# Optimization experiments

Hardware: AMD Instinct MI355X
Metric: run time of the kernel (lower is better)

## Reference

```python
import jax, jax.numpy as jnp
import numpy as np

# Fixed generation configuration (original samples num_nodes per graph from
# dataset stats; here batched with fixed node count so shapes are static).
B, N = 64, 384                 # num_graphs, nodes per graph
NOISE, CED, HID, FEAT, NCLS = 128, 64, 512, 256, 10
DENSITY = 0.05                 # fallback density used by the original code
TEMP = 1.0                     # temperature
IU, JU = np.triu_indices(N, k=1)   # all i<j pairs, matches nested loop order
P = IU.shape[0]                # pairs per graph = N*(N-1)/2
K = int(round(DENSITY * P))    # topk edges per graph


def setup_inputs() -> dict:
    key = jax.random.key(0)
    ks = jax.random.split(key, 8)
    f32 = jnp.float32
    return {
        "z": jax.random.normal(ks[0], (B, N, NOISE), f32),
        "class_labels": jax.random.randint(ks[1], (B,), 0, NCLS),
        "embed_table": jax.random.normal(ks[2], (NCLS, CED), f32),
        "W1": jax.random.normal(ks[3], (NOISE + CED, HID), f32) / np.float32(np.sqrt(NOISE + CED)),
        "b1": jnp.zeros((HID,), f32),
        "W2": jax.random.normal(ks[4], (HID, FEAT), f32) / np.float32(np.sqrt(HID)),
        "b2": jnp.zeros((FEAT,), f32),
        "We": jax.random.normal(ks[5], (FEAT, HID), f32) / np.float32(np.sqrt(FEAT)),
        "be": jnp.zeros((HID,), f32),
        "threshold": jnp.float32(1.0),
    }


def reference(z, class_labels, embed_table, W1, b1, W2, b2, We, be, threshold):
    # class embedding, broadcast to every node of the graph
    ce = embed_table[class_labels]                               # [B, CED]
    ce = jnp.broadcast_to(ce[:, None, :], (B, N, CED))
    inp = jnp.concatenate([z, ce], axis=-1)                      # [B, N, NOISE+CED]
    # node generator: Linear -> ReLU -> Linear
    x = jax.nn.relu(inp @ W1 + b1) @ W2 + b2                     # [B, N, FEAT]
    # edge predictor encoder: Linear -> ReLU
    h = jax.nn.relu(x @ We + be)                                 # [B, N, HID]
    # pairwise L2 distances via gram trick (replaces O(n^2) torch.norm loop)
    sq = jnp.sum(h * h, axis=-1)                                 # [B, N]
    gram = jnp.einsum('bnd,bmd->bnm', h, h)                      # [B, N, N]
    d2 = jnp.maximum(sq[:, :, None] + sq[:, None, :] - 2.0 * gram, 0.0)
    dist = jnp.sqrt(jnp.maximum(d2[:, IU, JU], 1e-12))           # [B, P] upper-tri pairs
    probs = jax.nn.sigmoid((threshold - dist) / max(TEMP, 1e-6)) # [B, P]
    # per-graph top-k edge selection
    top_probs, top_idx = jax.lax.top_k(probs, K)                 # [B, K]
    iu = jnp.asarray(IU, jnp.int32)
    ju = jnp.asarray(JU, jnp.int32)
    offs = (jnp.arange(B, dtype=jnp.int32) * N)[:, None]         # node offset per graph
    u = iu[top_idx] + offs                                       # [B, K]
    v = ju[top_idx] + offs
    # per graph: [[u, v], [v, u]] (symmetrized), graphs concatenated
    row0 = jnp.concatenate([u, v], axis=1).reshape(-1)           # [B*2K]
    row1 = jnp.concatenate([v, u], axis=1).reshape(-1)
    edge_index = jnp.stack([row0, row1], axis=0)                 # [2, B*2K]
    batch = jnp.repeat(jnp.arange(B, dtype=jnp.int32), N)        # [B*N]
    return x.reshape(B * N, FEAT), edge_index, batch, top_probs
```

## Files before the change

### kernel.cpp

```cpp
#include <hip/hip_runtime.h>
#include <hip/hip_bf16.h>

#define NB    64
#define NN    384
#define PPAIR 73536
#define PRECT 147456
#define KSEL  3677
#define NSLICE 8
#define SLICEK (PRECT / NSLICE)

#define OFF_X 0
#define OFF_E 6291456
#define B2K   470656
#define OFF_B 7232768
#define OFF_P 7257344
#define TOT   7492672

#define WS_H8    0ull
#define WS_GH    0ull
#define WS_SB    4194304ull
#define WS_SQ    12582912ull
#define WS_W1P   12681216ull
#define WS_W2P   12877824ull
#define WS_WEP   13139968ull
#define WS_KEY   13402112ull
#define WS_TB    39509248ull

typedef __attribute__((ext_vector_type(8))) short bf16x8;
typedef __attribute__((ext_vector_type(4))) float f32x4;

__device__ __forceinline__ short f2bf(float f) {
    __hip_bfloat16 h = __float2bfloat16(f);
    return *reinterpret_cast<short*>(&h);
}
__device__ __forceinline__ unsigned enc8(float h) {
    if (!(h > 0.0078125f)) return 0u;
    unsigned u = __float_as_uint(h) + 0x00080000u;
    int E = (int)(u >> 23) - 127;
    if (E > 8)  return 0x7Eu;
    if (E < -6) return 0u;
    return (unsigned)(((E + 7) << 3) | ((u >> 20) & 7u));
}
__device__ __forceinline__ float dec8(unsigned b) {
    if (b == 0u) return 0.f;
    return __uint_as_float((((b >> 3) + 120u) << 23) | ((b & 7u) << 20));
}

__device__ __forceinline__ void bar_lds() {
    asm volatile("s_waitcnt lgkmcnt(0)\n\ts_barrier" ::: "memory");
}

__device__ __forceinline__ int2 pack4bf(float a, float b, float c, float d) {
    int2 pk;
    pk.x = (unsigned short)f2bf(a) | ((unsigned)(unsigned short)f2bf(b) << 16);
    pk.y = (unsigned short)f2bf(c) | ((unsigned)(unsigned short)f2bf(d) << 16);
    return pk;
}

__device__ __forceinline__ void packOne(
    const float* __restrict__ W, int K, int N, short* __restrict__ dst, int idx)
{
    if (idx >= K * N) return;
    int j = idx & 7;
    int l = (idx >> 3) & 63;
    int rest = idx >> 9;
    int Kt = K >> 5;
    int kt = rest % Kt, mt = rest / Kt;
    int k = kt * 32 + (l >> 4) * 8 + j;
    int n = mt * 16 + (l & 15);
    dst[idx] = f2bf(W[(size_t)k * N + n]);
}

__global__ __launch_bounds__(256) void pack_all_kernel(
    const float* __restrict__ W1, const float* __restrict__ W2,
    const float* __restrict__ We, short* __restrict__ W1p,
    short* __restrict__ W2p, short* __restrict__ Wep, float* __restrict__ sqW)
{
    int blk = blockIdx.x, tid = threadIdx.x;
    if (blk < 384)        packOne(W1, 192, 512, W1p, blk * 256 + tid);
    else if (blk < 896)   packOne(W2, 512, 256, W2p, (blk - 384) * 256 + tid);
    else if (blk < 1408)  packOne(We, 256, 512, Wep, (blk - 896) * 256 + tid);
    else {
        int i = (blk - 1408) * 256 + tid;
        if (i < NB * NN) sqW[i] = 0.f;
    }
}

__global__ __launch_bounds__(512, 6) void fused_mlp_kernel(
    const float* __restrict__ z, const int* __restrict__ cls,
    const float* __restrict__ et,
    const short* __restrict__ W1p, const float* __restrict__ b1,
    const short* __restrict__ W2p, const float* __restrict__ b2,
    const short* __restrict__ Wep, const float* __restrict__ be,
    float* __restrict__ xOut, unsigned char* __restrict__ h8Out,
    float* __restrict__ sqOut)
{
    __shared__ short lds[23040];
    short* A_lds  = lds;
    short* t1_lds = lds + 6400;
    short* x_lds  = lds;

    const int tid = threadIdx.x;
    const int r0 = blockIdx.x * 32;
    const int lane = tid & 63;
    const int l15 = lane & 15, kj = lane >> 4;
    const int w = tid >> 6;
    const int cl = cls[r0 / NN];

    {
        float4 v[3];
#pragma unroll
        for (int q = 0; q < 3; ++q) {
            int u = tid + q * 512;
            int row = u / 48, c4 = u - row * 48;
            int col = c4 * 4;
            const float* src = (col < 128)
                ? (z + (size_t)(r0 + row) * 128 + col)
                : (et + cl * 64 + (col - 128));
            v[q] = *(const float4*)src;
        }
#pragma unroll
        for (int q = 0; q < 3; ++q) {
            int u = tid + q * 512;
            int row = u / 48, c4 = u - row * 48;
            *(int2*)(A_lds + row * 200 + c4 * 4) =
                pack4bf(v[q].x, v[q].y, v[q].z, v[q].w);
        }
    }
    bar_lds();

    {
        f32x4 acc1[4][2];
#pragma unroll
        for (int m = 0; m < 4; ++m)
#pragma unroll
            for (int s = 0; s < 2; ++s) acc1[m][s] = (f32x4){0.f, 0.f, 0.f, 0.f};

#pragma unroll
        for (int kt = 0; kt < 6; ++kt) {
            bf16x8 bF[2];
#pragma unroll
            for (int s = 0; s < 2; ++s)
                bF[s] = *(const bf16x8*)(A_lds + (s * 16 + l15) * 200 + kt * 32 + (kj << 3));
#pragma unroll
            for (int m = 0; m < 4; ++m) {
                int mt = w * 4 + m;
                bf16x8 aF = *(const bf16x8*)(W1p + ((size_t)(mt * 6 + kt) << 9) + (lane << 3));
#pragma unroll
                for (int s = 0; s < 2; ++s)
                    acc1[m][s] = __builtin_amdgcn_mfma_f32_16x16x32_bf16(aF, bF[s], acc1[m][s], 0, 0, 0);
            }
        }
#pragma unroll
        for (int m = 0; m < 4; ++m) {
            int fl = (w * 4 + m) * 16 + (kj << 2);
            float4 bv = *(const float4*)(b1 + fl);
#pragma unroll
            for (int s = 0; s < 2; ++s) {
                int node = s * 16 + l15;
                f32x4 a = acc1[m][s];
                float v0 = fmaxf(a.x + bv.x, 0.f), v1 = fmaxf(a.y + bv.y, 0.f);
                float v2 = fmaxf(a.z + bv.z, 0.f), v3 = fmaxf(a.w + bv.w, 0.f);
                *(int2*)(t1_lds + node * 520 + fl) = pack4bf(v0, v1, v2, v3);
            }
        }
    }
    bar_lds();

    f32x4 acc2[2][2];
#pragma unroll
    for (int t = 0; t < 2; ++t)
#pragma unroll
        for (int s = 0; s < 2; ++s) acc2[t][s] = (f32x4){0.f, 0.f, 0.f, 0.f};

#pragma unroll
    for (int kt = 0; kt < 16; ++kt) {
        bf16x8 bF[2];
#pragma unroll
        for (int s = 0; s < 2; ++s)
            bF[s] = *(const bf16x8*)(t1_lds + (s * 16 + l15) * 520 + kt * 32 + (kj << 3));
#pragma unroll
        for (int t = 0; t < 2; ++t) {
            int mt = w * 2 + t;
            bf16x8 aF = *(const bf16x8*)(W2p + ((size_t)(mt * 16 + kt) << 9) + (lane << 3));
#pragma unroll
            for (int s = 0; s < 2; ++s)
                acc2[t][s] = __builtin_amdgcn_mfma_f32_16x16x32_bf16(aF, bF[s], acc2[t][s], 0, 0, 0);
        }
    }
    bar_lds();

#pragma unroll
    for (int t = 0; t < 2; ++t) {
        int feat = (w * 2 + t) * 16 + (kj << 2);
        float4 bv = *(const float4*)(b2 + feat);
#pragma unroll
        for (int s = 0; s < 2; ++s) {
            int node = s * 16 + l15;
            f32x4 a = acc2[t][s];
            float v0 = a.x + bv.x, v1 = a.y + bv.y;
            float v2 = a.z + bv.z, v3 = a.w + bv.w;
            float4 o; o.x = v0; o.y = v1; o.z = v2; o.w = v3;
            *(float4*)(xOut + (size_t)(r0 + node) * 256 + feat) = o;
            *(int2*)(x_lds + node * 264 + feat) = pack4bf(v0, v1, v2, v3);
        }
    }
    bar_lds();

    {
        f32x4 acc3[4][2];
#pragma unroll
        for (int m = 0; m < 4; ++m)
#pragma unroll
            for (int s = 0; s < 2; ++s) acc3[m][s] = (f32x4){0.f, 0.f, 0.f, 0.f};

#pragma unroll
        for (int kt = 0; kt < 8; ++kt) {
            bf16x8 bF[2];
#pragma unroll
            for (int s = 0; s < 2; ++s)
                bF[s] = *(const bf16x8*)(x_lds + (s * 16 + l15) * 264 + kt * 32 + (kj << 3));
#pragma unroll
            for (int m = 0; m < 4; ++m) {
                int mt = w * 4 + m;
                bf16x8 aF = *(const bf16x8*)(Wep + ((size_t)(mt * 8 + kt) << 9) + (lane << 3));
#pragma unroll
                for (int s = 0; s < 2; ++s)
                    acc3[m][s] = __builtin_amdgcn_mfma_f32_16x16x32_bf16(aF, bF[s], acc3[m][s], 0, 0, 0);
            }
        }
        float sqp[2] = {0.f, 0.f};
#pragma unroll
        for (int m = 0; m < 4; ++m) {
            int feat = (w * 4 + m) * 16 + (kj << 2);
            float4 bv = *(const float4*)(be + feat);
#pragma unroll
            for (int s = 0; s < 2; ++s) {
                int node = s * 16 + l15;
                f32x4 a = acc3[m][s];
                float v0 = fmaxf(a.x + bv.x, 0.f), v1 = fmaxf(a.y + bv.y, 0.f);
                float v2 = fmaxf(a.z + bv.z, 0.f), v3 = fmaxf(a.w + bv.w, 0.f);
                unsigned e0 = enc8(v0), e1 = enc8(v1), e2 = enc8(v2), e3 = enc8(v3);
                *(unsigned*)(h8Out + (size_t)(r0 + node) * 512 + feat) =
                    e0 | (e1 << 8) | (e2 << 16) | (e3 << 24);
                float h0 = dec8(e0), h1 = dec8(e1), h2 = dec8(e2), h3 = dec8(e3);
                sqp[s] += h0 * h0 + h1 * h1 + h2 * h2 + h3 * h3;
            }
        }
#pragma unroll
        for (int s = 0; s < 2; ++s) {
            float v = sqp[s];
            v += __shfl_xor(v, 16);
            v += __shfl_xor(v, 32);
            if (kj == 0)
                atomicAdd(sqOut + r0 + s * 16 + l15, v);
        }
    }
}

__global__ __launch_bounds__(256) void gram_mfma_kernel(
    const unsigned char* __restrict__ hW8, const float* __restrict__ sqW,
    unsigned short* __restrict__ keyW)
{
    extern __shared__ unsigned char smem8[];
    unsigned char* As = smem8;
    unsigned char* Bs = smem8 + 16896;

    const int tid = threadIdx.x;
    const int b  = blockIdx.x;
    int tp = blockIdx.y;
    int ti = 0; { int rem = tp; while (rem >= 6 - ti) { rem -= 6 - ti; ++ti; } tp = rem; }
    const int tj = ti + tp;
    const bool diag = (ti == tj);
    const unsigned char* Bp = diag ? As : Bs;

    const int w = tid >> 6;
    const int lane = tid & 63;
    const int l15 = lane & 15, kj = lane >> 4;
    const int mb = w * 16;

    f32x4 acc[4];
#pragma unroll
    for (int t = 0; t < 4; ++t) acc[t] = (f32x4){0.f, 0.f, 0.f, 0.f};

    const size_t baseA = ((size_t)b * NN + ti * 64) * 512;
    const size_t baseB = ((size_t)b * NN + tj * 64) * 512;

    int4 pa[4], pb[4];
    auto issue = [&](int kc) {
#pragma unroll
        for (int q = 0; q < 4; ++q) {
            int i = tid + (q << 8);
            int row = i >> 4, g = i & 15;
            pa[q] = *(const int4*)(hW8 + baseA + row * 512 + kc * 256 + g * 16);
            if (!diag)
                pb[q] = *(const int4*)(hW8 + baseB + row * 512 + kc * 256 + g * 16);
        }
    };
    auto store = [&]() {
#pragma unroll
        for (int q = 0; q < 4; ++q) {
            int i = tid + (q << 8);
            int row = i >> 4, g = i & 15;
            *(int4*)(As + row * 264 + g * 16) = pa[q];
            if (!diag) *(int4*)(Bs + row * 264 + g * 16) = pb[q];
        }
    };

    issue(0);
    for (int kc = 0; kc < 2; ++kc) {
        store();
        if (kc == 0) issue(1);
        bar_lds();
#pragma unroll
        for (int kt = 0; kt < 8; ++kt) {
            long long aF = *(const long long*)(As + (mb + l15) * 264 + kt * 32 + kj * 8);
#pragma unroll
            for (int nt = 0; nt < 4; ++nt) {
                long long bF = *(const long long*)(Bp + (nt * 16 + l15) * 264 + kt * 32 + kj * 8);
                acc[nt] = __builtin_amdgcn_mfma_f32_16x16x32_fp8_fp8(aF, bF, acc[nt], 0, 0, 0);
            }
        }
        bar_lds();
    }

    unsigned short* tile = (unsigned short*)smem8;
    float4 sqi = *(const float4*)(sqW + b * NN + ti * 64 + mb + kj * 4);
    float si[4] = { sqi.x, sqi.y, sqi.z, sqi.w };
#pragma unroll
    for (int nt = 0; nt < 4; ++nt) {
        int colL = nt * 16 + l15;
        float sj = sqW[b * NN + tj * 64 + colL];
        float av[4] = { acc[nt].x, acc[nt].y, acc[nt].z, acc[nt].w };
#pragma unroll
        for (int r = 0; r < 4; ++r) {
            int rowL = mb + kj * 4 + r;
            float d2 = fmaxf(si[r] + sj - 2.f * av[r], 0.f);
            unsigned short key = (unsigned short)(__float_as_uint(d2) >> 16);
            bool valid = !diag || (rowL < colL);
            tile[rowL * 72 + colL] = valid ? key : (unsigned short)0xFFFF;
        }
    }
    bar_lds();
#pragma unroll
    for (int it = 0; it < 2; ++it) {
        int idx = tid + (it << 8);
        int row = idx >> 3, c8 = idx & 7;
        int4 v = *(const int4*)(tile + row * 72 + c8 * 8);
        *(int4*)(keyW + (size_t)b * PRECT + (size_t)(ti * 64 + row) * NN
                 + tj * 64 + c8 * 8) = v;
    }
}

__global__ __launch_bounds__(1024) void selA_kernel(
    const unsigned short* __restrict__ keyW, unsigned short* __restrict__ ghist)
{
    const int b = blockIdx.x, s = blockIdx.y, tid = threadIdx.x;
    const unsigned short* keys = keyW + (size_t)b * PRECT + (size_t)s * SLICEK;
    __shared__ unsigned hist[4096];
    for (int i = tid; i < 4096; i += 1024) hist[i] = 0;
    __syncthreads();
    for (int p = tid; p < SLICEK; p += 1024) {
        unsigned k = keys[p];
        if (k < 0x8000u) atomicAdd(&hist[k >> 4], 1u);
    }
    __syncthreads();
    unsigned short* dst = ghist + ((size_t)(b * NSLICE + s) << 12);
    for (int i = tid; i < 4096; i += 1024) dst[i] = (unsigned short)hist[i];
}

__global__ __launch_bounds__(1024) void selB_kernel(
    const unsigned short* __restrict__ ghist, unsigned* __restrict__ sliceBase,
    unsigned* __restrict__ Tbuf, float* __restrict__ outF)
{
    const int b = blockIdx.x, tid = threadIdx.x;
    __shared__ unsigned base[4096];
    __shared__ unsigned scanBuf[1024];
    __shared__ int sTc;
    if (tid == 0) sTc = 4095;

    unsigned c[4]; unsigned tsum = 0;
#pragma unroll
    for (int q = 0; q < 4; ++q) {
        int bin = tid * 4 + q;
        unsigned v = 0;
        for (int s = 0; s < NSLICE; ++s)
            v += ghist[((size_t)(b * NSLICE + s) << 12) + bin];
        c[q] = v; tsum += v;
    }
    scanBuf[tid] = tsum;
    __syncthreads();
    for (int o = 1; o < 1024; o <<= 1) {
        unsigned v = (tid >= o) ? scanBuf[tid - o] : 0u;
        __syncthreads();
        scanBuf[tid] += v;
        __syncthreads();
    }
    unsigned exc = scanBuf[tid] - tsum;
    {
        unsigned run = exc;
#pragma unroll
        for (int q = 0; q < 4; ++q) { base[tid * 4 + q] = run; run += c[q]; }
    }
    __syncthreads();
#pragma unroll
    for (int q = 0; q < 4; ++q) {
        int i = tid * 4 + q;
        if (base[i] < KSEL && base[i] + c[q] >= KSEL) atomicMin(&sTc, i);
    }
    __syncthreads();
    if (tid == 0) Tbuf[b] = (unsigned)sTc;

#pragma unroll
    for (int q = 0; q < 4; ++q) {
        int bin = tid * 4 + q;
        unsigned runb = base[bin];
        for (int s = 0; s < NSLICE; ++s) {
            size_t off = ((size_t)(b * NSLICE + s) << 12) + bin;
            sliceBase[off] = runb;
            runb += ghist[off];
        }
    }
    for (int i = tid; i < NN; i += 1024)
        outF[OFF_B + (size_t)b * NN + i] = (float)b;
}

__global__ __launch_bounds__(1024) void selC_emit_kernel(
    const unsigned short* __restrict__ keyW, const unsigned* __restrict__ sliceBase,
    const unsigned* __restrict__ Tbuf, const float* __restrict__ thrp,
    float* __restrict__ outF)
{
    const int b = blockIdx.x, s = blockIdx.y, tid = threadIdx.x;
    const unsigned short* keys = keyW + (size_t)b * PRECT + (size_t)s * SLICEK;
    __shared__ unsigned cnt[4096];
    const unsigned* src = sliceBase + ((size_t)(b * NSLICE + s) << 12);
    for (int i = tid; i < 4096; i += 1024) cnt[i] = src[i];
    __syncthreads();
    const int T = (int)Tbuf[b];
    const float thr0 = thrp[0];
    float* eb = outF + OFF_E + (size_t)b * (2 * KSEL);
    for (int p = tid; p < SLICEK; p += 1024) {
        unsigned k = keys[p];
        if (k < 0x8000u) {
            int bin = k >> 4;
            if (bin <= T) {
                unsigned pos = atomicAdd(&cnt[bin], 1u);
                if (pos < KSEL) {
                    int pg = s * SLICEK + p;
                    int i = pg / NN;
                    int j = pg - i * NN;
                    float u = (float)(b * NN + i);
                    float v = (float)(b * NN + j);
                    eb[pos] = u;
                    eb[KSEL + pos] = v;
                    eb[B2K + pos] = v;
                    eb[B2K + KSEL + pos] = u;
                    float d2 = __uint_as_float(((unsigned)k) << 16);
                    float dist = sqrtf(fmaxf(d2, 1e-12f));
                    outF[OFF_P + (size_t)b * KSEL + pos] =
                        1.0f / (1.0f + expf(dist - thr0));
                }
            }
        }
    }
}

extern "C" void kernel_launch(void* const* d_in, const int* in_sizes, int n_in,
                              void* d_out, int out_size, void* d_ws, size_t ws_size,
                              hipStream_t stream) {
    (void)in_sizes; (void)n_in; (void)out_size; (void)ws_size;
    const float* z   = (const float*)d_in[0];
    const int*   cls = (const int*)d_in[1];
    const float* et  = (const float*)d_in[2];
    const float* W1  = (const float*)d_in[3];
    const float* b1  = (const float*)d_in[4];
    const float* W2  = (const float*)d_in[5];
    const float* b2  = (const float*)d_in[6];
    const float* We  = (const float*)d_in[7];
    const float* be  = (const float*)d_in[8];
    const float* thr = (const float*)d_in[9];
    float* outF = (float*)d_out;

    char* w = (char*)d_ws;
    unsigned char*  hW8   = (unsigned char*)(w + WS_H8);
    float*          sqW   = (float*)(w + WS_SQ);
    short*          W1p   = (short*)(w + WS_W1P);
    short*          W2p   = (short*)(w + WS_W2P);
    short*          Wep   = (short*)(w + WS_WEP);
    unsigned short* keyW  = (unsigned short*)(w + WS_KEY);
    unsigned short* ghist = (unsigned short*)(w + WS_GH);
    unsigned*       sbase = (unsigned*)(w + WS_SB);
    unsigned*       Tbuf  = (unsigned*)(w + WS_TB);

    pack_all_kernel<<<1504, 256, 0, stream>>>(W1, W2, We, W1p, W2p, Wep, sqW);

    fused_mlp_kernel<<<768, 512, 0, stream>>>(
        z, cls, et, W1p, b1, W2p, b2, Wep, be, outF + OFF_X, hW8, sqW);

    gram_mfma_kernel<<<dim3(64, 21), 256, 33792, stream>>>(hW8, sqW, keyW);
    selA_kernel<<<dim3(64, NSLICE), 1024, 0, stream>>>(keyW, ghist);
    selB_kernel<<<64, 1024, 0, stream>>>(ghist, sbase, Tbuf, outF);
    selC_emit_kernel<<<dim3(64, NSLICE), 1024, 0, stream>>>(
        keyW, sbase, Tbuf, thr, outF);
}
```

Baseline: 201.4 us.

## Fuse histogram build into gram kernel and use global per-graph bin counters

```diff
diff --git a/kernel.cpp b/kernel.cpp
--- a/kernel.cpp
+++ b/kernel.cpp
@@ -17,14 +17,14 @@
 #define TOT   7492672
 
 #define WS_H8    0ull
-#define WS_GH    0ull
-#define WS_SB    4194304ull
 #define WS_SQ    12582912ull
 #define WS_W1P   12681216ull
 #define WS_W2P   12877824ull
 #define WS_WEP   13139968ull
 #define WS_KEY   13402112ull
-#define WS_TB    39509248ull
+#define WS_GH32  32276480ull
+#define WS_GC    33325056ull
+#define WS_TB    34373632ull
 
 typedef __attribute__((ext_vector_type(8))) short bf16x8;
 typedef __attribute__((ext_vector_type(4))) float f32x4;
@@ -74,15 +74,19 @@
 __global__ __launch_bounds__(256) void pack_all_kernel(
     const float* __restrict__ W1, const float* __restrict__ W2,
     const float* __restrict__ We, short* __restrict__ W1p,
-    short* __restrict__ W2p, short* __restrict__ Wep, float* __restrict__ sqW)
+    short* __restrict__ W2p, short* __restrict__ Wep,
+    float* __restrict__ sqW, unsigned* __restrict__ ghist32)
 {
     int blk = blockIdx.x, tid = threadIdx.x;
     if (blk < 384)        packOne(W1, 192, 512, W1p, blk * 256 + tid);
     else if (blk < 896)   packOne(W2, 512, 256, W2p, (blk - 384) * 256 + tid);
     else if (blk < 1408)  packOne(We, 256, 512, Wep, (blk - 896) * 256 + tid);
-    else {
+    else if (blk < 1504) {
         int i = (blk - 1408) * 256 + tid;
         if (i < NB * NN) sqW[i] = 0.f;
+    } else {
+        int i = (blk - 1504) * 256 + tid;
+        if (i < NB * 4096) ghist32[i] = 0u;
     }
 }
 
@@ -260,7 +264,7 @@
 
 __global__ __launch_bounds__(256) void gram_mfma_kernel(
     const unsigned char* __restrict__ hW8, const float* __restrict__ sqW,
-    unsigned short* __restrict__ keyW)
+    unsigned short* __restrict__ keyW, unsigned* __restrict__ ghist32)
 {
     extern __shared__ unsigned char smem8[];
     unsigned char* As = smem8;
@@ -325,6 +329,10 @@
     }
 
     unsigned short* tile = (unsigned short*)smem8;
+    unsigned* hist = (unsigned*)(smem8 + 16896);
+    for (int i = tid; i < 4096; i += 256) hist[i] = 0;
+    bar_lds();
+
     float4 sqi = *(const float4*)(sqW + b * NN + ti * 64 + mb + kj * 4);
     float si[4] = { sqi.x, sqi.y, sqi.z, sqi.w };
 #pragma unroll
@@ -339,6 +347,8 @@
             unsigned short key = (unsigned short)(__float_as_uint(d2) >> 16);
             bool valid = !diag || (rowL < colL);
             tile[rowL * 72 + colL] = valid ? key : (unsigned short)0xFFFF;
+            if (valid && key < (unsigned short)0x8000u)
+                atomicAdd(&hist[key >> 4], 1u);
         }
     }
     bar_lds();
@@ -350,27 +360,14 @@
         *(int4*)(keyW + (size_t)b * PRECT + (size_t)(ti * 64 + row) * NN
                  + tj * 64 + c8 * 8) = v;
     }
-}
-
-__global__ __launch_bounds__(1024) void selA_kernel(
-    const unsigned short* __restrict__ keyW, unsigned short* __restrict__ ghist)
-{
-    const int b = blockIdx.x, s = blockIdx.y, tid = threadIdx.x;
-    const unsigned short* keys = keyW + (size_t)b * PRECT + (size_t)s * SLICEK;
-    __shared__ unsigned hist[4096];
-    for (int i = tid; i < 4096; i += 1024) hist[i] = 0;
-    __syncthreads();
-    for (int p = tid; p < SLICEK; p += 1024) {
-        unsigned k = keys[p];
-        if (k < 0x8000u) atomicAdd(&hist[k >> 4], 1u);
-    }
-    __syncthreads();
-    unsigned short* dst = ghist + ((size_t)(b * NSLICE + s) << 12);
-    for (int i = tid; i < 4096; i += 1024) dst[i] = (unsigned short)hist[i];
+    for (int i = tid; i < 4096; i += 256) {
+        unsigned v = hist[i];
+        if (v) atomicAdd(&ghist32[(size_t)b * 4096 + i], v);
+    }
 }
 
 __global__ __launch_bounds__(1024) void selB_kernel(
-    const unsigned short* __restrict__ ghist, unsigned* __restrict__ sliceBase,
+    const unsigned* __restrict__ ghist32, unsigned* __restrict__ gcnt,
     unsigned* __restrict__ Tbuf, float* __restrict__ outF)
 {
     const int b = blockIdx.x, tid = threadIdx.x;
@@ -383,9 +380,7 @@
 #pragma unroll
     for (int q = 0; q < 4; ++q) {
         int bin = tid * 4 + q;
-        unsigned v = 0;
-        for (int s = 0; s < NSLICE; ++s)
-            v += ghist[((size_t)(b * NSLICE + s) << 12) + bin];
+        unsigned v = ghist32[(size_t)b * 4096 + bin];
         c[q] = v; tsum += v;
     }
     scanBuf[tid] = tsum;
@@ -414,30 +409,22 @@
 #pragma unroll
     for (int q = 0; q < 4; ++q) {
         int bin = tid * 4 + q;
-        unsigned runb = base[bin];
-        for (int s = 0; s < NSLICE; ++s) {
-            size_t off = ((size_t)(b * NSLICE + s) << 12) + bin;
-            sliceBase[off] = runb;
-            runb += ghist[off];
-        }
+        gcnt[(size_t)b * 4096 + bin] = base[bin];
     }
     for (int i = tid; i < NN; i += 1024)
         outF[OFF_B + (size_t)b * NN + i] = (float)b;
 }
 
 __global__ __launch_bounds__(1024) void selC_emit_kernel(
-    const unsigned short* __restrict__ keyW, const unsigned* __restrict__ sliceBase,
+    const unsigned short* __restrict__ keyW, unsigned* __restrict__ gcnt,
     const unsigned* __restrict__ Tbuf, const float* __restrict__ thrp,
     float* __restrict__ outF)
 {
     const int b = blockIdx.x, s = blockIdx.y, tid = threadIdx.x;
     const unsigned short* keys = keyW + (size_t)b * PRECT + (size_t)s * SLICEK;
-    __shared__ unsigned cnt[4096];
-    const unsigned* src = sliceBase + ((size_t)(b * NSLICE + s) << 12);
-    for (int i = tid; i < 4096; i += 1024) cnt[i] = src[i];
-    __syncthreads();
     const int T = (int)Tbuf[b];
     const float thr0 = thrp[0];
+    unsigned* cnt = gcnt + (size_t)b * 4096;
     float* eb = outF + OFF_E + (size_t)b * (2 * KSEL);
     for (int p = tid; p < SLICEK; p += 1024) {
         unsigned k = keys[p];
@@ -488,18 +475,18 @@
     short*          W2p   = (short*)(w + WS_W2P);
     short*          Wep   = (short*)(w + WS_WEP);
     unsigned short* keyW  = (unsigned short*)(w + WS_KEY);
-    unsigned short* ghist = (unsigned short*)(w + WS_GH);
-    unsigned*       sbase = (unsigned*)(w + WS_SB);
+    unsigned*       gh32  = (unsigned*)(w + WS_GH32);
+    unsigned*       gcnt  = (unsigned*)(w + WS_GC);
     unsigned*       Tbuf  = (unsigned*)(w + WS_TB);
 
-    pack_all_kernel<<<1504, 256, 0, stream>>>(W1, W2, We, W1p, W2p, Wep, sqW);
+    pack_all_kernel<<<2528, 256, 0, stream>>>(W1, W2, We, W1p, W2p, Wep, sqW, gh32);
 
     fused_mlp_kernel<<<768, 512, 0, stream>>>(
         z, cls, et, W1p, b1, W2p, b2, Wep, be, outF + OFF_X, hW8, sqW);
 
-    gram_mfma_kernel<<<dim3(64, 21), 256, 33792, stream>>>(hW8, sqW, keyW);
-    selA_kernel<<<dim3(64, NSLICE), 1024, 0, stream>>>(keyW, ghist);
-    selB_kernel<<<64, 1024, 0, stream>>>(ghist, sbase, Tbuf, outF);
+    gram_mfma_kernel<<<dim3(64, 21), 256, 33792, stream>>>(hW8, sqW, keyW, gh32);
+
+    selB_kernel<<<64, 1024, 0, stream>>>(gh32, gcnt, Tbuf, outF);
     selC_emit_kernel<<<dim3(64, NSLICE), 1024, 0, stream>>>(
-        keyW, sbase, Tbuf, thr, outF);
-}
+        keyW, gcnt, Tbuf, thr, outF);
+}
```

New measurement: 293.7 us. 1.46x slower.

## Load full K in one stage and split gram tile across eight waves

Applied to the files above, without the earlier changes.

```diff
diff --git a/kernel.cpp b/kernel.cpp
--- a/kernel.cpp
+++ b/kernel.cpp
@@ -258,13 +258,13 @@
     }
 }
 
-__global__ __launch_bounds__(256) void gram_mfma_kernel(
+__global__ __launch_bounds__(512) void gram_mfma_kernel(
     const unsigned char* __restrict__ hW8, const float* __restrict__ sqW,
     unsigned short* __restrict__ keyW)
 {
     extern __shared__ unsigned char smem8[];
     unsigned char* As = smem8;
-    unsigned char* Bs = smem8 + 16896;
+    unsigned char* Bs = smem8 + 33280;
 
     const int tid = threadIdx.x;
     const int b  = blockIdx.x;
@@ -274,67 +274,61 @@
     const bool diag = (ti == tj);
     const unsigned char* Bp = diag ? As : Bs;
 
-    const int w = tid >> 6;
     const int lane = tid & 63;
     const int l15 = lane & 15, kj = lane >> 4;
-    const int mb = w * 16;
-
-    f32x4 acc[4];
-#pragma unroll
-    for (int t = 0; t < 4; ++t) acc[t] = (f32x4){0.f, 0.f, 0.f, 0.f};
+    const int w = tid >> 6;
+    const int mbr = (w & 3) * 16;
+    const int mbc = (w >> 2) * 32;
+
+    f32x4 acc[2];
+#pragma unroll
+    for (int t = 0; t < 2; ++t) acc[t] = (f32x4){0.f, 0.f, 0.f, 0.f};
 
     const size_t baseA = ((size_t)b * NN + ti * 64) * 512;
     const size_t baseB = ((size_t)b * NN + tj * 64) * 512;
 
-    int4 pa[4], pb[4];
-    auto issue = [&](int kc) {
+    {
+        int4 pa[4], pb[4];
 #pragma unroll
         for (int q = 0; q < 4; ++q) {
-            int i = tid + (q << 8);
-            int row = i >> 4, g = i & 15;
-            pa[q] = *(const int4*)(hW8 + baseA + row * 512 + kc * 256 + g * 16);
+            int u = tid + (q << 9);
+            int row = u >> 5, g = u & 31;
+            pa[q] = *(const int4*)(hW8 + baseA + row * 512 + g * 16);
             if (!diag)
-                pb[q] = *(const int4*)(hW8 + baseB + row * 512 + kc * 256 + g * 16);
-        }
-    };
-    auto store = [&]() {
+                pb[q] = *(const int4*)(hW8 + baseB + row * 512 + g * 16);
+        }
 #pragma unroll
         for (int q = 0; q < 4; ++q) {
-            int i = tid + (q << 8);
-            int row = i >> 4, g = i & 15;
-            *(int4*)(As + row * 264 + g * 16) = pa[q];
-            if (!diag) *(int4*)(Bs + row * 264 + g * 16) = pb[q];
-        }
-    };
-
-    issue(0);
-    for (int kc = 0; kc < 2; ++kc) {
-        store();
-        if (kc == 0) issue(1);
-        bar_lds();
-#pragma unroll
-        for (int kt = 0; kt < 8; ++kt) {
-            long long aF = *(const long long*)(As + (mb + l15) * 264 + kt * 32 + kj * 8);
-#pragma unroll
-            for (int nt = 0; nt < 4; ++nt) {
-                long long bF = *(const long long*)(Bp + (nt * 16 + l15) * 264 + kt * 32 + kj * 8);
-                acc[nt] = __builtin_amdgcn_mfma_f32_16x16x32_fp8_fp8(aF, bF, acc[nt], 0, 0, 0);
-            }
-        }
-        bar_lds();
-    }
+            int u = tid + (q << 9);
+            int row = u >> 5, g = u & 31;
+            *(int4*)(As + row * 520 + g * 16) = pa[q];
+            if (!diag) *(int4*)(Bs + row * 520 + g * 16) = pb[q];
+        }
+    }
+    bar_lds();
+
+#pragma unroll
+    for (int kt = 0; kt < 16; ++kt) {
+        long long aF = *(const long long*)(As + (mbr + l15) * 520 + kt * 32 + kj * 8);
+#pragma unroll
+        for (int nt = 0; nt < 2; ++nt) {
+            long long bF = *(const long long*)(Bp + (mbc + nt * 16 + l15) * 520 + kt * 32 + kj * 8);
+            acc[nt] = __builtin_amdgcn_mfma_f32_16x16x32_fp8_fp8(aF, bF, acc[nt], 0, 0, 0);
+        }
+    }
+    bar_lds();
 
     unsigned short* tile = (unsigned short*)smem8;
-    float4 sqi = *(const float4*)(sqW + b * NN + ti * 64 + mb + kj * 4);
+    float4 sqi = *(const float4*)(sqW + b * NN + ti * 64 + mbr + kj * 4);
     float si[4] = { sqi.x, sqi.y, sqi.z, sqi.w };
 #pragma unroll
-    for (int nt = 0; nt < 4; ++nt) {
-        int colL = nt * 16 + l15;
+    for (int nt = 0; nt < 2; ++nt) {
+        int colL = mbc + nt * 16 + l15;
         float sj = sqW[b * NN + tj * 64 + colL];
         float av[4] = { acc[nt].x, acc[nt].y, acc[nt].z, acc[nt].w };
 #pragma unroll
         for (int r = 0; r < 4; ++r) {
-            int rowL = mb + kj * 4 + r;
+            int rowL = mbr + kj * 4 + r;
             float d2 = fmaxf(si[r] + sj - 2.f * av[r], 0.f);
             unsigned short key = (unsigned short)(__float_as_uint(d2) >> 16);
             bool valid = !diag || (rowL < colL);
@@ -342,9 +336,8 @@
         }
     }
     bar_lds();
-#pragma unroll
-    for (int it = 0; it < 2; ++it) {
-        int idx = tid + (it << 8);
+    {
+        int idx = tid;
         int row = idx >> 3, c8 = idx & 7;
         int4 v = *(const int4*)(tile + row * 72 + c8 * 8);
         *(int4*)(keyW + (size_t)b * PRECT + (size_t)(ti * 64 + row) * NN
@@ -497,7 +490,8 @@
     fused_mlp_kernel<<<768, 512, 0, stream>>>(
         z, cls, et, W1p, b1, W2p, b2, Wep, be, outF + OFF_X, hW8, sqW);
 
-    gram_mfma_kernel<<<dim3(64, 21), 256, 33792, stream>>>(hW8, sqW, keyW);
+    gram_mfma_kernel<<<dim3(64, 21), 512, 66560, stream>>>(hW8, sqW, keyW);
+
     selA_kernel<<<dim3(64, NSLICE), 1024, 0, stream>>>(keyW, ghist);
     selB_kernel<<<64, 1024, 0, stream>>>(ghist, sbase, Tbuf, outF);
     selC_emit_kernel<<<dim3(64, NSLICE), 1024, 0, stream>>>(
```

New measurement: 189.4 us. 6.0% less time.
